# Kernel optimization log

Hardware: AMD Instinct MI355X
Metric: run time of the kernel (lower is better)

## Reference

```python
import jax, jax.numpy as jnp
import numpy as np

EPS = 1e-5


def setup_inputs() -> dict:
    key = jax.random.key(0)
    ks = jax.random.split(key, 5)
    N, E, D, L = 10000, 160000, 512, 3
    x = jax.random.normal(ks[0], (N, D), dtype=jnp.float32)
    src = jax.random.randint(ks[1], (E,), 0, N, dtype=jnp.int64)
    dst = jax.random.randint(ks[2], (E,), 0, N, dtype=jnp.int64)
    gamma = jnp.ones((L, D), dtype=jnp.float32)
    beta = jnp.zeros((L, D), dtype=jnp.float32)
    # glorot-ish scale so ReLU stack stays well-conditioned
    W = jax.random.normal(ks[3], (L, D, D), dtype=jnp.float32) * (1.0 / np.sqrt(D))
    b = jnp.zeros((L, D), dtype=jnp.float32)
    return {"x": x, "src": src, "dst": dst, "gamma": gamma, "beta": beta, "W": W, "b": b}


def reference(x, src, dst, gamma, beta, W, b):
    N = x.shape[0]
    ones = jnp.ones(src.shape[0], dtype=x.dtype)
    # DGL GraphConv norm='both': src side uses out-degree, dst side uses in-degree
    out_deg = jnp.clip(jax.ops.segment_sum(ones, src, num_segments=N), 1.0)
    in_deg = jnp.clip(jax.ops.segment_sum(ones, dst, num_segments=N), 1.0)
    src_norm = (out_deg ** -0.5)[:, None]  # [N,1]
    dst_norm = (in_deg ** -0.5)[:, None]   # [N,1]
    n_layers = gamma.shape[0]
    for i in range(n_layers):
        # BatchNorm1d (training mode: batch mean, biased variance)
        mu = jnp.mean(x, axis=0)
        var = jnp.var(x, axis=0)
        x = (x - mu) * jax.lax.rsqrt(var + EPS) * gamma[i] + beta[i]
        h = x * src_norm
        agg = jax.ops.segment_sum(h[src], dst, num_segments=N) * dst_norm
        x = jax.nn.relu(agg @ W[i] + b[i])
    return x
```

## Files before the change

### kernel.cpp

```cpp
#include <hip/hip_runtime.h>
#include <hip/hip_bf16.h>

constexpr int N = 10000;
constexpr int D = 512;
constexpr int E = 160000;
constexpr int L = 3;
constexpr float EPS = 1e-5f;

typedef _Float16 half8 __attribute__((ext_vector_type(8)));
typedef _Float16 half2v __attribute__((ext_vector_type(2)));
typedef float floatx4 __attribute__((ext_vector_type(4)));

__device__ __forceinline__ void glds16(const _Float16* g, _Float16* l) {
    __builtin_amdgcn_global_load_lds(
        (const __attribute__((address_space(1))) uint32_t*)(g),
        (__attribute__((address_space(3))) uint32_t*)(l),
        16, 0, 0);
}

constexpr int CONV_BLOCKS = 250;
constexpr int DEG_BLOCKS  = (E + 255) / 256;
constexpr int TW_BLOCKS   = L * 256;
constexpr int MEGA_BLOCKS = CONV_BLOCKS + DEG_BLOCKS + TW_BLOCKS;

__global__ __launch_bounds__(256) void mega_setup(
    const int* __restrict__ src, const int* __restrict__ dst,
    const float* __restrict__ x, const float* __restrict__ W,
    int* __restrict__ out_deg, int* __restrict__ in_deg,
    _Float16* __restrict__ x16, float* __restrict__ stats0,
    _Float16* __restrict__ Wt) {
    __shared__ float tb[32][33];
    int bid = blockIdx.x;
    int tid = threadIdx.x;
    if (bid < CONV_BLOCKS) {
        int r0 = bid * 40;
        int r1 = r0 + 40; if (r1 > N) r1 = N;
        int c2 = tid * 2;
        float s0 = 0.f, s1 = 0.f, q0 = 0.f, q1 = 0.f;
        for (int r = r0; r < r1; ++r) {
            float2 v = *(const float2*)(x + (size_t)r * D + c2);
            s0 += v.x; q0 += v.x * v.x;
            s1 += v.y; q1 += v.y * v.y;
            half2v h; h[0] = (_Float16)v.x; h[1] = (_Float16)v.y;
            *(half2v*)(x16 + (size_t)r * D + c2) = h;
        }
        atomicAdd(&stats0[c2], s0);
        atomicAdd(&stats0[c2 + 1], s1);
        atomicAdd(&stats0[D + c2], q0);
        atomicAdd(&stats0[D + c2 + 1], q1);
    } else if (bid < CONV_BLOCKS + DEG_BLOCKS) {
        int e = (bid - CONV_BLOCKS) * 256 + tid;
        if (e < E) {
            atomicAdd(&out_deg[src[e]], 1);
            atomicAdd(&in_deg[dst[e]], 1);
        }
    } else {
        int b = bid - CONV_BLOCKS - DEG_BLOCKS;
        int l = b >> 8;
        int t = b & 255;
        int k0 = (t >> 4) * 32, n0 = (t & 15) * 32;
        int tx = tid & 31, ty = tid >> 5;
        const float* Wl = W + (size_t)l * D * D;
        _Float16* Wtl = Wt + (size_t)l * D * D;
        for (int i = 0; i < 32; i += 8)
            tb[ty + i][tx] = Wl[(size_t)(k0 + ty + i) * D + n0 + tx];
        __syncthreads();
        for (int i = 0; i < 32; i += 8)
            Wtl[(size_t)(n0 + ty + i) * D + k0 + tx] = (_Float16)tb[tx][ty + i];
    }
}

__global__ void scan_indeg(const int* __restrict__ in_deg,
                           const int* __restrict__ out_deg,
                           int* __restrict__ off, int* __restrict__ cursor,
                           float* __restrict__ src_norm, float* __restrict__ dst_norm) {
    __shared__ int lsum[1024];
    int t = threadIdx.x;
    const int chunk = (N + 1023) / 1024;
    int start = t * chunk;
    int end = start + chunk; if (end > N) end = N;
    int s = 0;
    for (int i = start; i < end; ++i) s += in_deg[i];
    lsum[t] = s;
    __syncthreads();
    for (int d = 1; d < 1024; d <<= 1) {
        int v = (t >= d) ? lsum[t - d] : 0;
        __syncthreads();
        lsum[t] += v;
        __syncthreads();
    }
    int excl = (t == 0) ? 0 : lsum[t - 1];
    for (int i = start; i < end; ++i) {
        off[i] = excl;
        cursor[i] = excl;
        excl += in_deg[i];
        int od = out_deg[i]; if (od < 1) od = 1;
        int id = in_deg[i];  if (id < 1) id = 1;
        src_norm[i] = rsqrtf((float)od);
        dst_norm[i] = rsqrtf((float)id);
    }
    if (t == 1023) off[N] = lsum[1023];
}

__global__ void csr_fill(const int* __restrict__ src, const int* __restrict__ dst,
                         int* __restrict__ cursor, int* __restrict__ csr_src,
                         float* __restrict__ csr_norm,
                         const float* __restrict__ src_norm) {
    int e = blockIdx.x * blockDim.x + threadIdx.x;
    if (e >= E) return;
    int s = src[e];
    int d = dst[e];
    int pos = atomicAdd(&cursor[d], 1);
    csr_src[pos] = s;
    csr_norm[pos] = src_norm[s];
}

__global__ __launch_bounds__(256) void aggregate_bn(
    const _Float16* __restrict__ x, const int* __restrict__ off,
    const int* __restrict__ csr_src, const float* __restrict__ csr_norm,
    const float* __restrict__ dst_norm, const float* __restrict__ stats,
    const float* __restrict__ gamma, const float* __restrict__ beta,
    _Float16* __restrict__ agg) {
    int wid = (blockIdx.x * 256 + threadIdx.x) >> 6;
    if (wid >= N) return;
    int lane = threadIdx.x & 63;
    int c0 = lane * 8;
    const _Float16* xp = x + c0;

    int e0 = __builtin_amdgcn_readfirstlane(off[wid]);
    int e1 = __builtin_amdgcn_readfirstlane(off[wid + 1]);

    float a[8] = {};
    float t = 0.f;
    int e = e0;
    for (; e + 8 <= e1; e += 8) {
        int s0 = csr_src[e + 0];
        int s1 = csr_src[e + 1];
        int s2 = csr_src[e + 2];
        int s3 = csr_src[e + 3];
        int s4 = csr_src[e + 4];
        int s5 = csr_src[e + 5];
        int s6 = csr_src[e + 6];
        int s7 = csr_src[e + 7];
        float n0 = csr_norm[e + 0];
        float n1 = csr_norm[e + 1];
        float n2 = csr_norm[e + 2];
        float n3 = csr_norm[e + 3];
        float n4 = csr_norm[e + 4];
        float n5 = csr_norm[e + 5];
        float n6 = csr_norm[e + 6];
        float n7 = csr_norm[e + 7];
        half8 v0 = *(const half8*)(xp + (size_t)s0 * D);
        half8 v1 = *(const half8*)(xp + (size_t)s1 * D);
        half8 v2 = *(const half8*)(xp + (size_t)s2 * D);
        half8 v3 = *(const half8*)(xp + (size_t)s3 * D);
        half8 v4 = *(const half8*)(xp + (size_t)s4 * D);
        half8 v5 = *(const half8*)(xp + (size_t)s5 * D);
        half8 v6 = *(const half8*)(xp + (size_t)s6 * D);
        half8 v7 = *(const half8*)(xp + (size_t)s7 * D);
        t += ((n0 + n1) + (n2 + n3)) + ((n4 + n5) + (n6 + n7));
#pragma unroll
        for (int k = 0; k < 8; ++k) {
            float p0 = (float)v0[k] * n0 + (float)v1[k] * n1;
            float p1 = (float)v2[k] * n2 + (float)v3[k] * n3;
            float p2 = (float)v4[k] * n4 + (float)v5[k] * n5;
            float p3 = (float)v6[k] * n6 + (float)v7[k] * n7;
            a[k] += (p0 + p1) + (p2 + p3);
        }
    }
    for (; e < e1; ++e) {
        int s0 = csr_src[e];
        float n0 = csr_norm[e];
        half8 v0 = *(const half8*)(xp + (size_t)s0 * D);
        t += n0;
#pragma unroll
        for (int k = 0; k < 8; ++k) a[k] += (float)v0[k] * n0;
    }

    float dn = dst_norm[wid];
    const float invN = 1.0f / (float)N;
    half8 o;
#pragma unroll
    for (int k = 0; k < 8; ++k) {
        int c = c0 + k;
        float mu = stats[c] * invN;
        float var = stats[D + c] * invN - mu * mu;
        float sc = gamma[c] * rsqrtf(var + EPS);
        float sh = beta[c] - mu * sc;
        o[k] = (_Float16)(dn * (sc * a[k] + sh * t));
    }
    *(half8*)(agg + (size_t)wid * D + c0) = o;
}

template <typename OutT, bool STATS>
__global__ __launch_bounds__(256) void mm_f16_relu(
    const _Float16* __restrict__ A, const _Float16* __restrict__ Bt,
    const float* __restrict__ bias, OutT* __restrict__ C, int M,
    float* __restrict__ stats) {
    __shared__ __align__(16) _Float16 As[2][128 * 64];
    __shared__ __align__(16) _Float16 Bs[2][128 * 64];
    const int tid  = threadIdx.x;
    const int wave = tid >> 6;
    const int lane = tid & 63;
    const int quad = lane >> 4;
    const int l16  = lane & 15;
    const int row0 = blockIdx.x * 128;
    const int col0 = blockIdx.y * 128;
    const int wm = (wave & 1) * 64;
    const int wn = (wave >> 1) * 64;

    const int srl = lane >> 3;
    const int sq  = lane & 7;
    const int sqs = (sq ^ srl) * 8;

    const _Float16* gA[4];
    const _Float16* gB[4];
#pragma unroll
    for (int j = 0; j < 4; ++j) {
        int ar = row0 + wave * 32 + j * 8 + srl;
        if (ar >= M) ar = M - 1;
        gA[j] = A + (size_t)ar * D + sqs;
        int br = col0 + wave * 32 + j * 8 + srl;
        gB[j] = Bt + (size_t)br * D + sqs;
    }

    const int l7 = l16 & 7;
    const int swz0 = (quad ^ l7) * 8;
    const int swz1 = ((4 + quad) ^ l7) * 8;

    floatx4 acc[4][4] = {};

    auto stage = [&](int buf, int k0) {
        _Float16* as = As[buf] + (wave * 32) * 64;
        _Float16* bs = Bs[buf] + (wave * 32) * 64;
#pragma unroll
        for (int j = 0; j < 4; ++j) {
            glds16(gA[j] + k0, as + j * 8 * 64);
            glds16(gB[j] + k0, bs + j * 8 * 64);
        }
    };

    stage(0, 0);
    __syncthreads();

    int cur = 0;
    for (int kt = 0; kt < 8; ++kt) {
        if (kt < 7) stage(cur ^ 1, (kt + 1) * 64);
        const _Float16* asb = As[cur];
        const _Float16* bsb = Bs[cur];
        half8 af0[4], af1[4], bf0[4], bf1[4];
#pragma unroll
        for (int i = 0; i < 4; ++i) {
            int r = wm + i * 16 + l16;
            af0[i] = *(const half8*)(asb + r * 64 + swz0);
            af1[i] = *(const half8*)(asb + r * 64 + swz1);
        }
#pragma unroll
        for (int j = 0; j < 4; ++j) {
            int r = wn + j * 16 + l16;
            bf0[j] = *(const half8*)(bsb + r * 64 + swz0);
            bf1[j] = *(const half8*)(bsb + r * 64 + swz1);
        }
#pragma unroll
        for (int i = 0; i < 4; ++i)
#pragma unroll
            for (int j = 0; j < 4; ++j)
                acc[i][j] = __builtin_amdgcn_mfma_f32_16x16x32_f16(
                    af0[i], bf0[j], acc[i][j], 0, 0, 0);
#pragma unroll
        for (int i = 0; i < 4; ++i)
#pragma unroll
            for (int j = 0; j < 4; ++j)
                acc[i][j] = __builtin_amdgcn_mfma_f32_16x16x32_f16(
                    af1[i], bf1[j], acc[i][j], 0, 0, 0);
        __syncthreads();
        cur ^= 1;
    }

    float s[4] = {}, q[4] = {};
    for (int i = 0; i < 4; ++i) {
        for (int r = 0; r < 4; ++r) {
            int row = row0 + wm + i * 16 + quad * 4 + r;
            bool valid = row < M;
            for (int j = 0; j < 4; ++j) {
                int col = col0 + wn + j * 16 + l16;
                float v = acc[i][j][r] + bias[col];
                v = v > 0.f ? v : 0.f;
                if (valid) {
                    C[(size_t)row * D + col] = (OutT)v;
                    if (STATS) { s[j] += v; q[j] += v * v; }
                }
            }
        }
    }
    if (STATS) {
        for (int j = 0; j < 4; ++j) {
            float sv = s[j], qv = q[j];
            sv += __shfl_xor(sv, 16); sv += __shfl_xor(sv, 32);
            qv += __shfl_xor(qv, 16); qv += __shfl_xor(qv, 32);
            if (quad == 0) {
                int col = col0 + wn + j * 16 + l16;
                atomicAdd(&stats[col], sv);
                atomicAdd(&stats[D + col], qv);
            }
        }
    }
}

extern "C" void kernel_launch(void* const* d_in, const int* in_sizes, int n_in,
                              void* d_out, int out_size, void* d_ws, size_t ws_size,
                              hipStream_t stream) {
    const float* x_in  = (const float*)d_in[0];
    const int*   src   = (const int*)d_in[1];
    const int*   dst   = (const int*)d_in[2];
    const float* gamma = (const float*)d_in[3];
    const float* beta  = (const float*)d_in[4];
    const float* W     = (const float*)d_in[5];
    const float* b     = (const float*)d_in[6];
    float* out = (float*)d_out;

    char* p = (char*)d_ws;
    _Float16* x16 = (_Float16*)p;  p += (size_t)N * D * 2;
    _Float16* agg = (_Float16*)p;  p += (size_t)N * D * 2;
    _Float16* Wt  = (_Float16*)p;  p += (size_t)L * D * D * 2;
    float* src_norm = (float*)p;   p += (size_t)N * 4;
    float* dst_norm = (float*)p;   p += (size_t)N * 4;
    float* csr_norm = (float*)p;   p += (size_t)E * 4;
    int* out_deg   = (int*)p;      p += (size_t)N * 4;
    int* in_deg    = (int*)p;      p += (size_t)N * 4;
    float* stats0  = (float*)p;    p += 2 * D * 4;
    float* stats1  = (float*)p;    p += 2 * D * 4;
    float* stats2  = (float*)p;    p += 2 * D * 4;
    int* csr_off   = (int*)p;      p += (size_t)(N + 1) * 4;
    int* cursor    = (int*)p;      p += (size_t)N * 4;
    int* csr_src   = (int*)p;      p += (size_t)E * 4;

    float* stats_in[3] = {stats0, stats1, stats2};

    hipMemsetAsync(out_deg, 0, (2 * (size_t)N + 6 * D) * sizeof(int), stream);
    mega_setup<<<MEGA_BLOCKS, 256, 0, stream>>>(src, dst, x_in, W,
                                                out_deg, in_deg, x16, stats0, Wt);
    scan_indeg<<<1, 1024, 0, stream>>>(in_deg, out_deg, csr_off, cursor,
                                       src_norm, dst_norm);
    csr_fill<<<DEG_BLOCKS, 256, 0, stream>>>(src, dst, cursor, csr_src,
                                             csr_norm, src_norm);

    dim3 mm_grid((N + 127) / 128, D / 128);
    const int agg_blocks = (N + 3) / 4;

    for (int l = 0; l < L; ++l) {
        const float* gl  = gamma + (size_t)l * D;
        const float* bl  = beta + (size_t)l * D;
        const _Float16* Wl = Wt + (size_t)l * D * D;
        const float* bil = b + (size_t)l * D;

        aggregate_bn<<<agg_blocks, 256, 0, stream>>>(
            x16, csr_off, csr_src, csr_norm, dst_norm, stats_in[l], gl, bl, agg);
        if (l == L - 1) {
            mm_f16_relu<float, false><<<mm_grid, 256, 0, stream>>>(
                agg, Wl, bil, out, N, nullptr);
        } else {
            mm_f16_relu<_Float16, true><<<mm_grid, 256, 0, stream>>>(
                agg, Wl, bil, x16, N, stats_in[l + 1]);
        }
    }
}
```

Measured before the change: 282.3 us.

## Split aggregation across feature shards and edge groups within each wave

The gather-aggregate kernel now launches four feature shards of 128 channels each. Within a wave, four lane groups each process a strided subset of the node's edges, and the partial sums are combined with cross-lane shuffles. This exposes more parallel gather requests per node and quadruples the block count to improve latency hiding. In exchange, CSR indices and norms are reread once per shard, and the shuffle reductions add work.

```diff
diff --git a/kernel.cpp b/kernel.cpp
--- a/kernel.cpp
+++ b/kernel.cpp
@@ -6,6 +6,10 @@
 constexpr int E = 160000;
 constexpr int L = 3;
 constexpr float EPS = 1e-5f;
+
+constexpr int NSH = 4;
+constexpr int SHC = D / NSH;
+constexpr int NODE_BLOCKS = N / 4;
 
 typedef _Float16 half8 __attribute__((ext_vector_type(8)));
 typedef _Float16 half2v __attribute__((ext_vector_type(2)));
@@ -115,81 +119,73 @@
     csr_norm[pos] = src_norm[s];
 }
 
-__global__ __launch_bounds__(256) void aggregate_bn(
+__global__ __launch_bounds__(256) void aggregate_bn4(
     const _Float16* __restrict__ x, const int* __restrict__ off,
     const int* __restrict__ csr_src, const float* __restrict__ csr_norm,
     const float* __restrict__ dst_norm, const float* __restrict__ stats,
     const float* __restrict__ gamma, const float* __restrict__ beta,
     _Float16* __restrict__ agg) {
-    int wid = (blockIdx.x * 256 + threadIdx.x) >> 6;
-    if (wid >= N) return;
-    int lane = threadIdx.x & 63;
-    int c0 = lane * 8;
+    int shard = blockIdx.x / NODE_BLOCKS;
+    int blk   = blockIdx.x - shard * NODE_BLOCKS;
+    int wid   = blk * 4 + (threadIdx.x >> 6);
+    int lane  = threadIdx.x & 63;
+    int eg    = lane >> 4;
+    int ch    = lane & 15;
+    int c0    = shard * SHC + ch * 8;
     const _Float16* xp = x + c0;
 
     int e0 = __builtin_amdgcn_readfirstlane(off[wid]);
     int e1 = __builtin_amdgcn_readfirstlane(off[wid + 1]);
 
-    float a[8] = {};
-    float t = 0.f;
-    int e = e0;
-    for (; e + 8 <= e1; e += 8) {
-        int s0 = csr_src[e + 0];
-        int s1 = csr_src[e + 1];
-        int s2 = csr_src[e + 2];
-        int s3 = csr_src[e + 3];
-        int s4 = csr_src[e + 4];
-        int s5 = csr_src[e + 5];
-        int s6 = csr_src[e + 6];
-        int s7 = csr_src[e + 7];
-        float n0 = csr_norm[e + 0];
-        float n1 = csr_norm[e + 1];
-        float n2 = csr_norm[e + 2];
-        float n3 = csr_norm[e + 3];
-        float n4 = csr_norm[e + 4];
-        float n5 = csr_norm[e + 5];
-        float n6 = csr_norm[e + 6];
-        float n7 = csr_norm[e + 7];
+    float a[8] = {}, b2[8] = {};
+    float tA = 0.f, tB = 0.f;
+    int e = e0 + eg;
+    for (; e + 4 < e1; e += 8) {
+        int s0 = csr_src[e];
+        int s1 = csr_src[e + 4];
+        float n0 = csr_norm[e];
+        float n1 = csr_norm[e + 4];
         half8 v0 = *(const half8*)(xp + (size_t)s0 * D);
         half8 v1 = *(const half8*)(xp + (size_t)s1 * D);
-        half8 v2 = *(const half8*)(xp + (size_t)s2 * D);
-        half8 v3 = *(const half8*)(xp + (size_t)s3 * D);
-        half8 v4 = *(const half8*)(xp + (size_t)s4 * D);
-        half8 v5 = *(const half8*)(xp + (size_t)s5 * D);
-        half8 v6 = *(const half8*)(xp + (size_t)s6 * D);
-        half8 v7 = *(const half8*)(xp + (size_t)s7 * D);
-        t += ((n0 + n1) + (n2 + n3)) + ((n4 + n5) + (n6 + n7));
+        tA += n0; tB += n1;
 #pragma unroll
         for (int k = 0; k < 8; ++k) {
-            float p0 = (float)v0[k] * n0 + (float)v1[k] * n1;
-            float p1 = (float)v2[k] * n2 + (float)v3[k] * n3;
-            float p2 = (float)v4[k] * n4 + (float)v5[k] * n5;
-            float p3 = (float)v6[k] * n6 + (float)v7[k] * n7;
-            a[k] += (p0 + p1) + (p2 + p3);
-        }
-    }
-    for (; e < e1; ++e) {
+            a[k]  += (float)v0[k] * n0;
+            b2[k] += (float)v1[k] * n1;
+        }
+    }
+    if (e < e1) {
         int s0 = csr_src[e];
         float n0 = csr_norm[e];
         half8 v0 = *(const half8*)(xp + (size_t)s0 * D);
-        t += n0;
+        tA += n0;
 #pragma unroll
         for (int k = 0; k < 8; ++k) a[k] += (float)v0[k] * n0;
     }
-
-    float dn = dst_norm[wid];
-    const float invN = 1.0f / (float)N;
-    half8 o;
+    float t = tA + tB;
+    t += __shfl_xor(t, 16);
+    t += __shfl_xor(t, 32);
 #pragma unroll
     for (int k = 0; k < 8; ++k) {
-        int c = c0 + k;
-        float mu = stats[c] * invN;
-        float var = stats[D + c] * invN - mu * mu;
-        float sc = gamma[c] * rsqrtf(var + EPS);
-        float sh = beta[c] - mu * sc;
-        o[k] = (_Float16)(dn * (sc * a[k] + sh * t));
-    }
-    *(half8*)(agg + (size_t)wid * D + c0) = o;
+        a[k] += b2[k];
+        a[k] += __shfl_xor(a[k], 16);
+        a[k] += __shfl_xor(a[k], 32);
+    }
+    if (eg == 0) {
+        float dn = dst_norm[wid];
+        const float invN = 1.0f / (float)N;
+        half8 o;
+#pragma unroll
+        for (int k = 0; k < 8; ++k) {
+            int c = c0 + k;
+            float mu = stats[c] * invN;
+            float var = stats[D + c] * invN - mu * mu;
+            float sc = gamma[c] * rsqrtf(var + EPS);
+            float sh = beta[c] - mu * sc;
+            o[k] = (_Float16)(dn * (sc * a[k] + sh * t));
+        }
+        *(half8*)(agg + (size_t)wid * D + c0) = o;
+    }
 }
 
 template <typename OutT, bool STATS>
@@ -346,7 +342,7 @@
                                              csr_norm, src_norm);
 
     dim3 mm_grid((N + 127) / 128, D / 128);
-    const int agg_blocks = (N + 3) / 4;
+    const int agg_blocks = NSH * NODE_BLOCKS;
 
     for (int l = 0; l < L; ++l) {
         const float* gl  = gamma + (size_t)l * D;
@@ -354,7 +350,7 @@
         const _Float16* Wl = Wt + (size_t)l * D * D;
         const float* bil = b + (size_t)l * D;
 
-        aggregate_bn<<<agg_blocks, 256, 0, stream>>>(
+        aggregate_bn4<<<agg_blocks, 256, 0, stream>>>(
             x16, csr_off, csr_src, csr_norm, dst_norm, stats_in[l], gl, bl, agg);
         if (l == L - 1) {
             mm_f16_relu<float, false><<<mm_grid, 256, 0, stream>>>(
```

Measured after the change: 301.4 us. 1.07x slower.
